# Kernel tuning notes

Measured on AMD Instinct MI355X. Metric: run time of the kernel, lower is better.

Reference implementation:

```python
import jax, jax.numpy as jnp
import numpy as np

N = 50000
NEG_SLOPE = 0.2  # PyG GATConv default negative_slope


def gat_conv(x, src, dst, W, a_src, a_dst, b, heads, out_dim, concat):
    # x: [N, F_in]; W: [F_in, heads*out_dim]; a_src/a_dst: [heads, out_dim]
    h = (x @ W).reshape(N, heads, out_dim)                      # [N,H,D]
    alpha_src = jnp.einsum('nhd,hd->nh', h, a_src)              # [N,H]
    alpha_dst = jnp.einsum('nhd,hd->nh', h, a_dst)              # [N,H]
    e = jax.nn.leaky_relu(alpha_src[src] + alpha_dst[dst], NEG_SLOPE)  # [E,H]
    # segment softmax over incoming edges of each destination node
    m = jax.ops.segment_max(e, dst, num_segments=N)             # [N,H]
    ex = jnp.exp(e - m[dst])
    denom = jax.ops.segment_sum(ex, dst, num_segments=N)        # [N,H]
    alpha = ex / (denom[dst] + 1e-16)                           # [E,H]
    msg = h[src] * alpha[:, :, None]                            # [E,H,D]
    out = jax.ops.segment_sum(msg, dst, num_segments=N)         # [N,H,D]
    out = out.reshape(N, heads * out_dim) if concat else out.mean(axis=1)
    return out + b


def setup_inputs() -> dict:
    key = jax.random.key(0)
    ks = jax.random.split(key, 14)
    E = 800000
    IN, HID, H, LAT = 128, 64, 4, 64

    def glorot(k, shape):
        fan = shape[0] + shape[-1]
        return jax.random.uniform(k, shape, jnp.float32, -1.0, 1.0) * np.sqrt(6.0 / fan)

    return {
        'x': jax.random.normal(ks[0], (N, IN), jnp.float32),
        'edge_index': jax.random.randint(ks[1], (2, E), 0, N, jnp.int64),
        'W1': glorot(ks[2], (IN, H * HID)),
        'a_src1': glorot(ks[3], (H, HID)),
        'a_dst1': glorot(ks[4], (H, HID)),
        'b1': jnp.zeros((H * HID,), jnp.float32),
        'W_mu': glorot(ks[5], (H * HID, LAT)),
        'a_src_mu': glorot(ks[6], (1, LAT)),
        'a_dst_mu': glorot(ks[7], (1, LAT)),
        'b_mu': jnp.zeros((LAT,), jnp.float32),
        'W_ls': glorot(ks[8], (H * HID, LAT)),
        'a_src_ls': glorot(ks[9], (1, LAT)),
        'a_dst_ls': glorot(ks[10], (1, LAT)),
        'b_ls': jnp.zeros((LAT,), jnp.float32),
    }


def reference(x, edge_index, W1, a_src1, a_dst1, b1,
              W_mu, a_src_mu, a_dst_mu, b_mu,
              W_ls, a_src_ls, a_dst_ls, b_ls):
    # PyG GATConv adds self-loops by default
    loops = jnp.arange(N, dtype=edge_index.dtype)
    src = jnp.concatenate([edge_index[0], loops])
    dst = jnp.concatenate([edge_index[1], loops])

    h = jax.nn.relu(gat_conv(x, src, dst, W1, a_src1, a_dst1, b1, 4, 64, True))
    mu = gat_conv(h, src, dst, W_mu, a_src_mu, a_dst_mu, b_mu, 1, 64, False)
    logstd = gat_conv(h, src, dst, W_ls, a_src_ls, a_dst_ls, b_ls, 1, 64, False)
    return (mu, logstd)
```

## Files before the change

### kernel.cpp

```cpp
#include <hip/hip_runtime.h>
#include <hip/hip_bf16.h>

#define NNODES 50000
#define MT 3125
#define NB 196
#define BCAP 5248
typedef __hip_bfloat16 bf16;
typedef __attribute__((ext_vector_type(8))) short bf16x8;
typedef __attribute__((ext_vector_type(4))) float f32x4;

__device__ __forceinline__ void unpack2(unsigned w, float& lo, float& hi){
  lo = __uint_as_float(w << 16);
  hi = __uint_as_float(w & 0xffff0000u);
}
__device__ __forceinline__ short f2bf(float f){
  union { __hip_bfloat16 h; short s; } u; u.h = __float2bfloat16(f); return u.s;
}
__device__ __forceinline__ float lrelu(float v){ return v > 0.f ? v : 0.2f * v; }

__global__ __launch_bounds__(256)
void cvt_w_k(const float* __restrict__ W1, const float* __restrict__ Wmu,
             const float* __restrict__ Wls, bf16x8* __restrict__ Bp1,
             bf16x8* __restrict__ Bp2){
  int t = blockIdx.x * 256 + threadIdx.x;
  if (t < 4096){
    int lane = t & 63, ct = (t >> 6) & 15, kt = t >> 10;
    int k0 = kt * 32 + (lane >> 4) * 8, col = ct * 16 + (lane & 15);
    bf16x8 o;
    #pragma unroll
    for (int j = 0; j < 8; j++) o[j] = f2bf(W1[(size_t)(k0 + j) * 256 + col]);
    Bp1[t] = o;
  } else if (t < 8192){
    int u = t - 4096;
    int lane = u & 63, ct = (u >> 6) & 7, kt = u >> 9;
    int k0 = kt * 32 + (lane >> 4) * 8, col = ct * 16 + (lane & 15);
    const float* W = (col < 64) ? Wmu : Wls;
    int cc = col & 63;
    bf16x8 o;
    #pragma unroll
    for (int j = 0; j < 8; j++) o[j] = f2bf(W[(size_t)(k0 + j) * 64 + cc]);
    Bp2[u] = o;
  }
}

__global__ __launch_bounds__(256)
void gemm1_mfma(const float* __restrict__ x, const bf16x8* __restrict__ Bp,
                const float* __restrict__ aS, const float* __restrict__ aD,
                bf16* __restrict__ Y, float* __restrict__ as1, float* __restrict__ ad1){
  int rt = blockIdx.x;
  int w = threadIdx.x >> 6, lane = threadIdx.x & 63;
  const float* xr = x + (size_t)(rt * 16 + (lane & 15)) * 128 + (lane >> 4) * 8;
  f32x4 z = {0.f, 0.f, 0.f, 0.f};
  f32x4 acc[4] = {z, z, z, z};
  for (int kt = 0; kt < 4; kt++){
    float4 v0 = *(const float4*)(xr + kt * 32);
    float4 v1 = *(const float4*)(xr + kt * 32 + 4);
    bf16x8 a;
    a[0] = f2bf(v0.x); a[1] = f2bf(v0.y); a[2] = f2bf(v0.z); a[3] = f2bf(v0.w);
    a[4] = f2bf(v1.x); a[5] = f2bf(v1.y); a[6] = f2bf(v1.z); a[7] = f2bf(v1.w);
    #pragma unroll
    for (int c = 0; c < 4; c++){
      bf16x8 b = Bp[(size_t)(kt * 16 + w * 4 + c) * 64 + lane];
      acc[c] = __builtin_amdgcn_mfma_f32_16x16x32_bf16(a, b, acc[c], 0, 0, 0);
    }
  }
  int row0 = rt * 16 + (lane >> 4) * 4;
  #pragma unroll
  for (int c = 0; c < 4; c++){
    int col = w * 64 + c * 16 + (lane & 15);
    #pragma unroll
    for (int i = 0; i < 4; i++)
      Y[(size_t)(row0 + i) * 256 + col] = __float2bfloat16(acc[c][i]);
  }
  float aSv[4], aDv[4];
  #pragma unroll
  for (int c = 0; c < 4; c++){
    int col = c * 16 + (lane & 15);
    aSv[c] = aS[w * 64 + col];
    aDv[c] = aD[w * 64 + col];
  }
  #pragma unroll
  for (int i = 0; i < 4; i++){
    float s1 = 0.f, s2 = 0.f;
    #pragma unroll
    for (int c = 0; c < 4; c++){
      s1 = fmaf(acc[c][i], aSv[c], s1);
      s2 = fmaf(acc[c][i], aDv[c], s2);
    }
    #pragma unroll
    for (int o = 1; o < 16; o <<= 1){
      s1 += __shfl_xor(s1, o);
      s2 += __shfl_xor(s2, o);
    }
    if ((lane & 15) == 0){
      int node = row0 + i;
      as1[node * 4 + w] = s1;
      ad1[node * 4 + w] = s2;
    }
  }
}

__global__ __launch_bounds__(256)
void gemm2_mfma(const bf16x8* __restrict__ Ap, const bf16x8* __restrict__ Bp,
                const float* __restrict__ aSmu, const float* __restrict__ aDmu,
                const float* __restrict__ aSls, const float* __restrict__ aDls,
                bf16* __restrict__ Y2,
                float* __restrict__ as2m, float* __restrict__ ad2m,
                float* __restrict__ as2l, float* __restrict__ ad2l){
  int w = threadIdx.x >> 6, lane = threadIdx.x & 63;
  int rt = blockIdx.x * 4 + w;
  if (rt >= MT) return;
  f32x4 z = {0.f, 0.f, 0.f, 0.f};
  f32x4 acc[8] = {z, z, z, z, z, z, z, z};
  for (int kt = 0; kt < 8; kt++){
    bf16x8 a = Ap[(size_t)(rt * 8 + kt) * 64 + lane];
    #pragma unroll
    for (int c = 0; c < 8; c++){
      bf16x8 b = Bp[(size_t)(kt * 8 + c) * 64 + lane];
      acc[c] = __builtin_amdgcn_mfma_f32_16x16x32_bf16(a, b, acc[c], 0, 0, 0);
    }
  }
  int row0 = rt * 16 + (lane >> 4) * 4;
  #pragma unroll
  for (int c = 0; c < 4; c++){
    int col = c * 16 + (lane & 15);
    #pragma unroll
    for (int i = 0; i < 4; i++){
      Y2[(size_t)(row0 + i) * 128 + col]       = __float2bfloat16(acc[c][i]);
      Y2[(size_t)(row0 + i) * 128 + 64 + col]  = __float2bfloat16(acc[4 + c][i]);
    }
  }
  float aSm[4], aDm[4], aSl[4], aDl[4];
  #pragma unroll
  for (int c = 0; c < 4; c++){
    int col = c * 16 + (lane & 15);
    aSm[c] = aSmu[col]; aDm[c] = aDmu[col];
    aSl[c] = aSls[col]; aDl[c] = aDls[col];
  }
  #pragma unroll
  for (int i = 0; i < 4; i++){
    float s1 = 0.f, s2 = 0.f, s3 = 0.f, s4 = 0.f;
    #pragma unroll
    for (int c = 0; c < 4; c++){
      s1 = fmaf(acc[c][i], aSm[c], s1);
      s2 = fmaf(acc[c][i], aDm[c], s2);
      s3 = fmaf(acc[4 + c][i], aSl[c], s3);
      s4 = fmaf(acc[4 + c][i], aDl[c], s4);
    }
    #pragma unroll
    for (int o = 1; o < 16; o <<= 1){
      s1 += __shfl_xor(s1, o);
      s2 += __shfl_xor(s2, o);
      s3 += __shfl_xor(s3, o);
      s4 += __shfl_xor(s4, o);
    }
    if ((lane & 15) == 0){
      int node = row0 + i;
      as2m[node] = s1; ad2m[node] = s2;
      as2l[node] = s3; ad2l[node] = s4;
    }
  }
}

__global__ __launch_bounds__(256)
void bscat_k(const int* __restrict__ ei, int E0, int Etot,
             int* __restrict__ bcnt, unsigned* __restrict__ buck){
  __shared__ int lh[NB];
  __shared__ int lbase[NB];
  for (int i = threadIdx.x; i < NB; i += 256) lh[i] = 0;
  __syncthreads();
  int base = blockIdx.x * 1024 + threadIdx.x;
  int sA[4], dA[4], rA[4];
  #pragma unroll
  for (int q = 0; q < 4; q++){
    int e = base + q * 256;
    sA[q] = -1;
    if (e < Etot){
      int s, d;
      if (e < E0){ s = ei[e]; d = ei[E0 + e]; } else { s = d = e - E0; }
      sA[q] = s; dA[q] = d;
      rA[q] = atomicAdd(&lh[d >> 8], 1);
    }
  }
  __syncthreads();
  for (int i = threadIdx.x; i < NB; i += 256)
    lbase[i] = lh[i] ? atomicAdd(&bcnt[i], lh[i]) : 0;
  __syncthreads();
  #pragma unroll
  for (int q = 0; q < 4; q++){
    if (sA[q] >= 0){
      int bk = dA[q] >> 8;
      buck[(size_t)bk * BCAP + lbase[bk] + rA[q]] =
          ((unsigned)(dA[q] & 255) << 16) | (unsigned)sA[q];
    }
  }
}

__global__ __launch_bounds__(256)
void bcsr_k(const unsigned* __restrict__ buck, const int* __restrict__ bcnt,
            int* __restrict__ offs, int* __restrict__ srcs, int n, int total){
  int b = blockIdx.x;
  __shared__ int eh[256];
  __shared__ int buf[256];
  int t = threadIdx.x;
  int bv = (t < NB) ? bcnt[t] : 0;
  buf[t] = bv; __syncthreads();
  int bacc = bv;
  for (int off = 1; off < 256; off <<= 1){
    int x = (t >= off) ? buf[t - off] : 0;
    __syncthreads();
    bacc += x; buf[t] = bacc; __syncthreads();
  }
  int gbase = (b == 0) ? 0 : buf[b - 1];
  int cntb  = bcnt[b];
  const unsigned* slab = buck + (size_t)b * BCAP;
  __syncthreads();
  eh[t] = 0;
  __syncthreads();
  for (int j = t; j < cntb; j += 256)
    atomicAdd(&eh[(slab[j] >> 16) & 255], 1);
  __syncthreads();
  int v = eh[t];
  buf[t] = v; __syncthreads();
  int acc = v;
  for (int off = 1; off < 256; off <<= 1){
    int x = (t >= off) ? buf[t - off] : 0;
    __syncthreads();
    acc += x; buf[t] = acc; __syncthreads();
  }
  int loff = acc - v;
  int node = b * 256 + t;
  if (node < n) offs[node] = gbase + loff;
  if (b == NB - 1 && t == 0) offs[n] = total;
  __syncthreads();
  eh[t] = loff;
  __syncthreads();
  for (int j = t; j < cntb; j += 256){
    unsigned val = slab[j];
    int dlo = (val >> 16) & 255;
    int rank = atomicAdd(&eh[dlo], 1);
    srcs[gbase + rank] = (int)(val & 0xffffu);
  }
}

__global__ __launch_bounds__(128)
void gat_aggr1_k(const int* __restrict__ offs, const int* __restrict__ srcs,
                 const float* __restrict__ as, const float* __restrict__ ad,
                 const bf16* __restrict__ h, const float* __restrict__ b,
                 bf16x8* __restrict__ Ap2, int n){
  int node = blockIdx.x * 2 + (threadIdx.x >> 6);
  if (node >= n) return;
  int lane = threadIdx.x & 63;
  int beg = offs[node], end = offs[node + 1];
  int hA = lane >> 4, iA = lane & 15;
  float advA = ad[node * 4 + hA];
  float m = -1e30f;
  for (int j = beg + iA; j < end; j += 16)
    m = fmaxf(m, lrelu(as[srcs[j] * 4 + hA] + advA));
  #pragma unroll
  for (int o = 1; o < 16; o <<= 1) m = fmaxf(m, __shfl_xor(m, o));
  int hP = (lane >> 3) & 3, oct = lane & 7, slot = lane >> 5;
  float mP   = __shfl(m, hP * 16);
  float advP = __shfl(advA, hP * 16);
  float s = 0.f;
  float acc[8];
  #pragma unroll
  for (int i = 0; i < 8; i++) acc[i] = 0.f;
  float p_cur = 0.f;
  uint4 dw_cur = make_uint4(0u, 0u, 0u, 0u);
  {
    int j = beg + slot;
    if (j < end){
      int si = srcs[j];
      dw_cur = *(const uint4*)(h + (size_t)si * 256 + hP * 64 + oct * 8);
      float e = lrelu(as[si * 4 + hP] + advP);
      p_cur = __expf(e - mP);
    }
  }
  for (int j0 = beg; j0 < end; j0 += 2){
    int jn = j0 + 2 + slot;
    float p_nxt = 0.f;
    uint4 dw_nxt = make_uint4(0u, 0u, 0u, 0u);
    if (jn < end){
      int si = srcs[jn];
      dw_nxt = *(const uint4*)(h + (size_t)si * 256 + hP * 64 + oct * 8);
      float e = lrelu(as[si * 4 + hP] + advP);
      p_nxt = __expf(e - mP);
    }
    s += p_cur;
    float lo, hi;
    unpack2(dw_cur.x, lo, hi); acc[0] = fmaf(lo, p_cur, acc[0]); acc[1] = fmaf(hi, p_cur, acc[1]);
    unpack2(dw_cur.y, lo, hi); acc[2] = fmaf(lo, p_cur, acc[2]); acc[3] = fmaf(hi, p_cur, acc[3]);
    unpack2(dw_cur.z, lo, hi); acc[4] = fmaf(lo, p_cur, acc[4]); acc[5] = fmaf(hi, p_cur, acc[5]);
    unpack2(dw_cur.w, lo, hi); acc[6] = fmaf(lo, p_cur, acc[6]); acc[7] = fmaf(hi, p_cur, acc[7]);
    p_cur = p_nxt;
    dw_cur = dw_nxt;
  }
  s += __shfl_xor(s, 32);
  #pragma unroll
  for (int i = 0; i < 8; i++) acc[i] += __shfl_xor(acc[i], 32);
  if (lane < 32){
    float inv = 1.f / (s + 1e-16f);
    bf16x8 o;
    #pragma unroll
    for (int i = 0; i < 8; i++){
      float vv = acc[i] * inv + b[lane * 8 + i];
      o[i] = f2bf(vv > 0.f ? vv : 0.f);
    }
    int kt = lane >> 2, g = lane & 3;
    int rt = node >> 4, r = node & 15;
    Ap2[(size_t)(rt * 8 + kt) * 64 + g * 16 + r] = o;
  }
}

__global__ __launch_bounds__(128)
void gat_aggr2_k(const int* __restrict__ offs, const int* __restrict__ srcs,
                 const float* __restrict__ as2m, const float* __restrict__ ad2m,
                 const float* __restrict__ as2l, const float* __restrict__ ad2l,
                 const bf16* __restrict__ h2,
                 const float* __restrict__ bmu, const float* __restrict__ bls,
                 float* __restrict__ outmu, float* __restrict__ outls, int n){
  int node = blockIdx.x * 2 + (threadIdx.x >> 6);
  if (node >= n) return;
  int lane = threadIdx.x & 63;
  int beg = offs[node], end = offs[node + 1];
  const float* asA = (lane >= 32) ? as2l : as2m;
  float advA = ((lane >= 32) ? ad2l : ad2m)[node];
  int iA = lane & 31;
  float m = -1e30f;
  for (int j = beg + iA; j < end; j += 32)
    m = fmaxf(m, lrelu(asA[srcs[j]] + advA));
  #pragma unroll
  for (int o = 1; o < 32; o <<= 1) m = fmaxf(m, __shfl_xor(m, o));
  int br = (lane >> 3) & 1, oct = lane & 7, slot = lane >> 4;
  float mP   = __shfl(m, br * 32);
  float advP = __shfl(advA, br * 32);
  const float* asP = br ? as2l : as2m;
  float s = 0.f;
  float acc[8];
  #pragma unroll
  for (int i = 0; i < 8; i++) acc[i] = 0.f;
  #pragma unroll 8
  for (int j0 = beg; j0 < end; j0 += 4){
    int j = j0 + slot;
    if (j < end){
      int si = srcs[j];
      float e = lrelu(asP[si] + advP);
      float p = __expf(e - mP);
      s += p;
      uint4 dw = *(const uint4*)(h2 + (size_t)si * 128 + br * 64 + oct * 8);
      float lo, hi;
      unpack2(dw.x, lo, hi); acc[0] = fmaf(lo, p, acc[0]); acc[1] = fmaf(hi, p, acc[1]);
      unpack2(dw.y, lo, hi); acc[2] = fmaf(lo, p, acc[2]); acc[3] = fmaf(hi, p, acc[3]);
      unpack2(dw.z, lo, hi); acc[4] = fmaf(lo, p, acc[4]); acc[5] = fmaf(hi, p, acc[5]);
      unpack2(dw.w, lo, hi); acc[6] = fmaf(lo, p, acc[6]); acc[7] = fmaf(hi, p, acc[7]);
    }
  }
  #pragma unroll
  for (int off = 16; off <= 32; off <<= 1){
    s += __shfl_xor(s, off);
    #pragma unroll
    for (int i = 0; i < 8; i++) acc[i] += __shfl_xor(acc[i], off);
  }
  if (lane < 16){
    float inv = 1.f / (s + 1e-16f);
    const float* bb = (lane >= 8) ? bls : bmu;
    float* out = (lane >= 8) ? outls : outmu;
    float v[8];
    #pragma unroll
    for (int i = 0; i < 8; i++) v[i] = acc[i] * inv + bb[oct * 8 + i];
    float* op = out + (size_t)node * 64 + oct * 8;
    *(float4*)op       = make_float4(v[0], v[1], v[2], v[3]);
    *(float4*)(op + 4) = make_float4(v[4], v[5], v[6], v[7]);
  }
}

extern "C" void kernel_launch(void* const* d_in, const int* in_sizes, int n_in,
                              void* d_out, int out_size, void* d_ws, size_t ws_size,
                              hipStream_t stream){
  const float* x    = (const float*)d_in[0];
  const int*   ei   = (const int*)d_in[1];
  const float* W1   = (const float*)d_in[2];
  const float* aS1  = (const float*)d_in[3];
  const float* aD1  = (const float*)d_in[4];
  const float* b1   = (const float*)d_in[5];
  const float* Wmu  = (const float*)d_in[6];
  const float* aSmu = (const float*)d_in[7];
  const float* aDmu = (const float*)d_in[8];
  const float* bmu  = (const float*)d_in[9];
  const float* Wls  = (const float*)d_in[10];
  const float* aSls = (const float*)d_in[11];
  const float* aDls = (const float*)d_in[12];
  const float* bls  = (const float*)d_in[13];

  const int N    = NNODES;
  const int E0   = in_sizes[1] / 2;
  const int Etot = E0 + N;

  float* ws = (float*)d_ws;
  bf16x8* Ap2  = (bf16x8*)(ws);
  bf16*   h1bf = (bf16*)(ws + 6400000);
  bf16*   h2   = (bf16*)(ws + 12800000);
  float*  as1  = ws + 16000000;
  float*  ad1  = ws + 16200000;
  float*  as2m = ws + 16400000;
  float*  ad2m = ws + 16450000;
  float*  as2l = ws + 16500000;
  float*  ad2l = ws + 16550000;
  int*      offs  = (int*)(ws + 16600000);
  int*      srcs  = (int*)(ws + 16650016);
  unsigned* buck  = (unsigned*)(ws + 17500016);
  int*      bcnt  = (int*)(ws + 18528640);
  bf16x8*   Bp1   = (bf16x8*)(ws + 18528912);
  bf16x8*   Bp2   = (bf16x8*)(ws + 18545296);

  float* outmu = (float*)d_out;
  float* outls = (float*)d_out + 3200000;

  const int egrid4 = (Etot + 1023) / 1024;

  hipMemsetAsync(bcnt, 0, 256 * sizeof(int), stream);
  bscat_k<<<egrid4, 256, 0, stream>>>(ei, E0, Etot, bcnt, buck);
  bcsr_k<<<NB, 256, 0, stream>>>(buck, bcnt, offs, srcs, N, Etot);

  cvt_w_k<<<32, 256, 0, stream>>>(W1, Wmu, Wls, Bp1, Bp2);

  gemm1_mfma<<<MT, 256, 0, stream>>>(x, Bp1, aS1, aD1, h1bf, as1, ad1);
  gat_aggr1_k<<<(N + 1) / 2, 128, 0, stream>>>(offs, srcs, as1, ad1, h1bf, b1, Ap2, N);

  gemm2_mfma<<<(MT + 3) / 4, 256, 0, stream>>>(Ap2, Bp2, aSmu, aDmu, aSls, aDls,
                                               h2, as2m, ad2m, as2l, ad2l);
  gat_aggr2_k<<<(N + 1) / 2, 128, 0, stream>>>(offs, srcs, as2m, ad2m, as2l, ad2l,
                                               h2, bmu, bls, outmu, outls, N);
}
```

Before: 213.3 us.

## Fold weight conversion into bucket scatter and use grid-stride aggregation kernels

Merges the weight bf16 conversion kernel into the edge-bucketing kernel as extra blocks, removing one launch. Both aggregation kernels become persistent grid-stride loops over nodes with a fixed grid of 4096 blocks instead of one block per two nodes. The software-pipelined prefetch in the layer-1 aggregation is replaced with a simpler unrolled loop. The unrolled loop may expose less load latency hiding than the explicit double buffering, and a fixed grid can balance uneven node degrees less well.

```diff
diff --git a/kernel.cpp b/kernel.cpp
--- a/kernel.cpp
+++ b/kernel.cpp
@@ -17,31 +17,6 @@
   union { __hip_bfloat16 h; short s; } u; u.h = __float2bfloat16(f); return u.s;
 }
 __device__ __forceinline__ float lrelu(float v){ return v > 0.f ? v : 0.2f * v; }
-
-__global__ __launch_bounds__(256)
-void cvt_w_k(const float* __restrict__ W1, const float* __restrict__ Wmu,
-             const float* __restrict__ Wls, bf16x8* __restrict__ Bp1,
-             bf16x8* __restrict__ Bp2){
-  int t = blockIdx.x * 256 + threadIdx.x;
-  if (t < 4096){
-    int lane = t & 63, ct = (t >> 6) & 15, kt = t >> 10;
-    int k0 = kt * 32 + (lane >> 4) * 8, col = ct * 16 + (lane & 15);
-    bf16x8 o;
-    #pragma unroll
-    for (int j = 0; j < 8; j++) o[j] = f2bf(W1[(size_t)(k0 + j) * 256 + col]);
-    Bp1[t] = o;
-  } else if (t < 8192){
-    int u = t - 4096;
-    int lane = u & 63, ct = (u >> 6) & 7, kt = u >> 9;
-    int k0 = kt * 32 + (lane >> 4) * 8, col = ct * 16 + (lane & 15);
-    const float* W = (col < 64) ? Wmu : Wls;
-    int cc = col & 63;
-    bf16x8 o;
-    #pragma unroll
-    for (int j = 0; j < 8; j++) o[j] = f2bf(W[(size_t)(k0 + j) * 64 + cc]);
-    Bp2[u] = o;
-  }
-}
 
 __global__ __launch_bounds__(256)
 void gemm1_mfma(const float* __restrict__ x, const bf16x8* __restrict__ Bp,
@@ -164,7 +139,32 @@
 
 __global__ __launch_bounds__(256)
 void bscat_k(const int* __restrict__ ei, int E0, int Etot,
-             int* __restrict__ bcnt, unsigned* __restrict__ buck){
+             int* __restrict__ bcnt, unsigned* __restrict__ buck, int sblocks,
+             const float* __restrict__ W1, const float* __restrict__ Wmu,
+             const float* __restrict__ Wls, bf16x8* __restrict__ Bp1,
+             bf16x8* __restrict__ Bp2){
+  if (blockIdx.x >= sblocks){
+    int t = (blockIdx.x - sblocks) * 256 + threadIdx.x;
+    if (t < 4096){
+      int lane = t & 63, ct = (t >> 6) & 15, kt = t >> 10;
+      int k0 = kt * 32 + (lane >> 4) * 8, col = ct * 16 + (lane & 15);
+      bf16x8 o;
+      #pragma unroll
+      for (int j = 0; j < 8; j++) o[j] = f2bf(W1[(size_t)(k0 + j) * 256 + col]);
+      Bp1[t] = o;
+    } else if (t < 8192){
+      int u = t - 4096;
+      int lane = u & 63, ct = (u >> 6) & 7, kt = u >> 9;
+      int k0 = kt * 32 + (lane >> 4) * 8, col = ct * 16 + (lane & 15);
+      const float* W = (col < 64) ? Wmu : Wls;
+      int cc = col & 63;
+      bf16x8 o;
+      #pragma unroll
+      for (int j = 0; j < 8; j++) o[j] = f2bf(W[(size_t)(k0 + j) * 64 + cc]);
+      Bp2[u] = o;
+    }
+    return;
+  }
   __shared__ int lh[NB];
   __shared__ int lbase[NB];
   for (int i = threadIdx.x; i < NB; i += 256) lh[i] = 0;
@@ -248,68 +248,54 @@
                  const float* __restrict__ as, const float* __restrict__ ad,
                  const bf16* __restrict__ h, const float* __restrict__ b,
                  bf16x8* __restrict__ Ap2, int n){
-  int node = blockIdx.x * 2 + (threadIdx.x >> 6);
-  if (node >= n) return;
   int lane = threadIdx.x & 63;
-  int beg = offs[node], end = offs[node + 1];
   int hA = lane >> 4, iA = lane & 15;
-  float advA = ad[node * 4 + hA];
-  float m = -1e30f;
-  for (int j = beg + iA; j < end; j += 16)
-    m = fmaxf(m, lrelu(as[srcs[j] * 4 + hA] + advA));
-  #pragma unroll
-  for (int o = 1; o < 16; o <<= 1) m = fmaxf(m, __shfl_xor(m, o));
   int hP = (lane >> 3) & 3, oct = lane & 7, slot = lane >> 5;
-  float mP   = __shfl(m, hP * 16);
-  float advP = __shfl(advA, hP * 16);
-  float s = 0.f;
-  float acc[8];
-  #pragma unroll
-  for (int i = 0; i < 8; i++) acc[i] = 0.f;
-  float p_cur = 0.f;
-  uint4 dw_cur = make_uint4(0u, 0u, 0u, 0u);
-  {
-    int j = beg + slot;
-    if (j < end){
-      int si = srcs[j];
-      dw_cur = *(const uint4*)(h + (size_t)si * 256 + hP * 64 + oct * 8);
-      float e = lrelu(as[si * 4 + hP] + advP);
-      p_cur = __expf(e - mP);
-    }
-  }
-  for (int j0 = beg; j0 < end; j0 += 2){
-    int jn = j0 + 2 + slot;
-    float p_nxt = 0.f;
-    uint4 dw_nxt = make_uint4(0u, 0u, 0u, 0u);
-    if (jn < end){
-      int si = srcs[jn];
-      dw_nxt = *(const uint4*)(h + (size_t)si * 256 + hP * 64 + oct * 8);
-      float e = lrelu(as[si * 4 + hP] + advP);
-      p_nxt = __expf(e - mP);
-    }
-    s += p_cur;
-    float lo, hi;
-    unpack2(dw_cur.x, lo, hi); acc[0] = fmaf(lo, p_cur, acc[0]); acc[1] = fmaf(hi, p_cur, acc[1]);
-    unpack2(dw_cur.y, lo, hi); acc[2] = fmaf(lo, p_cur, acc[2]); acc[3] = fmaf(hi, p_cur, acc[3]);
-    unpack2(dw_cur.z, lo, hi); acc[4] = fmaf(lo, p_cur, acc[4]); acc[5] = fmaf(hi, p_cur, acc[5]);
-    unpack2(dw_cur.w, lo, hi); acc[6] = fmaf(lo, p_cur, acc[6]); acc[7] = fmaf(hi, p_cur, acc[7]);
-    p_cur = p_nxt;
-    dw_cur = dw_nxt;
-  }
-  s += __shfl_xor(s, 32);
-  #pragma unroll
-  for (int i = 0; i < 8; i++) acc[i] += __shfl_xor(acc[i], 32);
-  if (lane < 32){
-    float inv = 1.f / (s + 1e-16f);
-    bf16x8 o;
-    #pragma unroll
-    for (int i = 0; i < 8; i++){
-      float vv = acc[i] * inv + b[lane * 8 + i];
-      o[i] = f2bf(vv > 0.f ? vv : 0.f);
-    }
-    int kt = lane >> 2, g = lane & 3;
-    int rt = node >> 4, r = node & 15;
-    Ap2[(size_t)(rt * 8 + kt) * 64 + g * 16 + r] = o;
+  for (int node = blockIdx.x * 2 + (threadIdx.x >> 6); node < n; node += gridDim.x * 2){
+    int beg = offs[node], end = offs[node + 1];
+    float advA = ad[node * 4 + hA];
+    float m = -1e30f;
+    for (int j = beg + iA; j < end; j += 16)
+      m = fmaxf(m, lrelu(as[srcs[j] * 4 + hA] + advA));
+    #pragma unroll
+    for (int o = 1; o < 16; o <<= 1) m = fmaxf(m, __shfl_xor(m, o));
+    float mP   = __shfl(m, hP * 16);
+    float advP = __shfl(advA, hP * 16);
+    float s = 0.f;
+    float acc[8];
+    #pragma unroll
+    for (int i = 0; i < 8; i++) acc[i] = 0.f;
+    #pragma unroll 8
+    for (int j0 = beg; j0 < end; j0 += 2){
+      int j = j0 + slot;
+      if (j < end){
+        int si = srcs[j];
+        float e = lrelu(as[si * 4 + hP] + advP);
+        float p = __expf(e - mP);
+        s += p;
+        uint4 dw = *(const uint4*)(h + (size_t)si * 256 + hP * 64 + oct * 8);
+        float lo, hi;
+        unpack2(dw.x, lo, hi); acc[0] = fmaf(lo, p, acc[0]); acc[1] = fmaf(hi, p, acc[1]);
+        unpack2(dw.y, lo, hi); acc[2] = fmaf(lo, p, acc[2]); acc[3] = fmaf(hi, p, acc[3]);
+        unpack2(dw.z, lo, hi); acc[4] = fmaf(lo, p, acc[4]); acc[5] = fmaf(hi, p, acc[5]);
+        unpack2(dw.w, lo, hi); acc[6] = fmaf(lo, p, acc[6]); acc[7] = fmaf(hi, p, acc[7]);
+      }
+    }
+    s += __shfl_xor(s, 32);
+    #pragma unroll
+    for (int i = 0; i < 8; i++) acc[i] += __shfl_xor(acc[i], 32);
+    if (lane < 32){
+      float inv = 1.f / (s + 1e-16f);
+      bf16x8 o;
+      #pragma unroll
+      for (int i = 0; i < 8; i++){
+        float vv = acc[i] * inv + b[lane * 8 + i];
+        o[i] = f2bf(vv > 0.f ? vv : 0.f);
+      }
+      int kt = lane >> 2, g = lane & 3;
+      int rt = node >> 4, r = node & 15;
+      Ap2[(size_t)(rt * 8 + kt) * 64 + g * 16 + r] = o;
+    }
   }
 }
 
@@ -320,58 +306,59 @@
                  const bf16* __restrict__ h2,
                  const float* __restrict__ bmu, const float* __restrict__ bls,
                  float* __restrict__ outmu, float* __restrict__ outls, int n){
-  int node = blockIdx.x * 2 + (threadIdx.x >> 6);
-  if (node >= n) return;
   int lane = threadIdx.x & 63;
-  int beg = offs[node], end = offs[node + 1];
+  int iA = lane & 31;
+  int br = (lane >> 3) & 1, oct = lane & 7, slot = lane >> 4;
   const float* asA = (lane >= 32) ? as2l : as2m;
-  float advA = ((lane >= 32) ? ad2l : ad2m)[node];
-  int iA = lane & 31;
-  float m = -1e30f;
-  for (int j = beg + iA; j < end; j += 32)
-    m = fmaxf(m, lrelu(asA[srcs[j]] + advA));
-  #pragma unroll
-  for (int o = 1; o < 32; o <<= 1) m = fmaxf(m, __shfl_xor(m, o));
-  int br = (lane >> 3) & 1, oct = lane & 7, slot = lane >> 4;
-  float mP   = __shfl(m, br * 32);
-  float advP = __shfl(advA, br * 32);
+  const float* adA = (lane >= 32) ? ad2l : ad2m;
   const float* asP = br ? as2l : as2m;
-  float s = 0.f;
-  float acc[8];
-  #pragma unroll
-  for (int i = 0; i < 8; i++) acc[i] = 0.f;
-  #pragma unroll 8
-  for (int j0 = beg; j0 < end; j0 += 4){
-    int j = j0 + slot;
-    if (j < end){
-      int si = srcs[j];
-      float e = lrelu(asP[si] + advP);
-      float p = __expf(e - mP);
-      s += p;
-      uint4 dw = *(const uint4*)(h2 + (size_t)si * 128 + br * 64 + oct * 8);
-      float lo, hi;
-      unpack2(dw.x, lo, hi); acc[0] = fmaf(lo, p, acc[0]); acc[1] = fmaf(hi, p, acc[1]);
-      unpack2(dw.y, lo, hi); acc[2] = fmaf(lo, p, acc[2]); acc[3] = fmaf(hi, p, acc[3]);
-      unpack2(dw.z, lo, hi); acc[4] = fmaf(lo, p, acc[4]); acc[5] = fmaf(hi, p, acc[5]);
-      unpack2(dw.w, lo, hi); acc[6] = fmaf(lo, p, acc[6]); acc[7] = fmaf(hi, p, acc[7]);
-    }
-  }
-  #pragma unroll
-  for (int off = 16; off <= 32; off <<= 1){
-    s += __shfl_xor(s, off);
-    #pragma unroll
-    for (int i = 0; i < 8; i++) acc[i] += __shfl_xor(acc[i], off);
-  }
-  if (lane < 16){
-    float inv = 1.f / (s + 1e-16f);
-    const float* bb = (lane >= 8) ? bls : bmu;
-    float* out = (lane >= 8) ? outls : outmu;
-    float v[8];
-    #pragma unroll
-    for (int i = 0; i < 8; i++) v[i] = acc[i] * inv + bb[oct * 8 + i];
-    float* op = out + (size_t)node * 64 + oct * 8;
-    *(float4*)op       = make_float4(v[0], v[1], v[2], v[3]);
-    *(float4*)(op + 4) = make_float4(v[4], v[5], v[6], v[7]);
+  for (int node = blockIdx.x * 2 + (threadIdx.x >> 6); node < n; node += gridDim.x * 2){
+    int beg = offs[node], end = offs[node + 1];
+    float advA = adA[node];
+    float m = -1e30f;
+    for (int j = beg + iA; j < end; j += 32)
+      m = fmaxf(m, lrelu(asA[srcs[j]] + advA));
+    #pragma unroll
+    for (int o = 1; o < 32; o <<= 1) m = fmaxf(m, __shfl_xor(m, o));
+    float mP   = __shfl(m, br * 32);
+    float advP = __shfl(advA, br * 32);
+    float s = 0.f;
+    float acc[8];
+    #pragma unroll
+    for (int i = 0; i < 8; i++) acc[i] = 0.f;
+    #pragma unroll 8
+    for (int j0 = beg; j0 < end; j0 += 4){
+      int j = j0 + slot;
+      if (j < end){
+        int si = srcs[j];
+        float e = lrelu(asP[si] + advP);
+        float p = __expf(e - mP);
+        s += p;
+        uint4 dw = *(const uint4*)(h2 + (size_t)si * 128 + br * 64 + oct * 8);
+        float lo, hi;
+        unpack2(dw.x, lo, hi); acc[0] = fmaf(lo, p, acc[0]); acc[1] = fmaf(hi, p, acc[1]);
+        unpack2(dw.y, lo, hi); acc[2] = fmaf(lo, p, acc[2]); acc[3] = fmaf(hi, p, acc[3]);
+        unpack2(dw.z, lo, hi); acc[4] = fmaf(lo, p, acc[4]); acc[5] = fmaf(hi, p, acc[5]);
+        unpack2(dw.w, lo, hi); acc[6] = fmaf(lo, p, acc[6]); acc[7] = fmaf(hi, p, acc[7]);
+      }
+    }
+    #pragma unroll
+    for (int off = 16; off <= 32; off <<= 1){
+      s += __shfl_xor(s, off);
+      #pragma unroll
+      for (int i = 0; i < 8; i++) acc[i] += __shfl_xor(acc[i], off);
+    }
+    if (lane < 16){
+      float inv = 1.f / (s + 1e-16f);
+      const float* bb = (lane >= 8) ? bls : bmu;
+      float* out = (lane >= 8) ? outls : outmu;
+      float v[8];
+      #pragma unroll
+      for (int i = 0; i < 8; i++) v[i] = acc[i] * inv + bb[oct * 8 + i];
+      float* op = out + (size_t)node * 64 + oct * 8;
+      *(float4*)op       = make_float4(v[0], v[1], v[2], v[3]);
+      *(float4*)(op + 4) = make_float4(v[4], v[5], v[6], v[7]);
+    }
   }
 }
 
@@ -420,16 +407,15 @@
   const int egrid4 = (Etot + 1023) / 1024;
 
   hipMemsetAsync(bcnt, 0, 256 * sizeof(int), stream);
-  bscat_k<<<egrid4, 256, 0, stream>>>(ei, E0, Etot, bcnt, buck);
+  bscat_k<<<egrid4 + 32, 256, 0, stream>>>(ei, E0, Etot, bcnt, buck, egrid4,
+                                           W1, Wmu, Wls, Bp1, Bp2);
   bcsr_k<<<NB, 256, 0, stream>>>(buck, bcnt, offs, srcs, N, Etot);
 
-  cvt_w_k<<<32, 256, 0, stream>>>(W1, Wmu, Wls, Bp1, Bp2);
-
   gemm1_mfma<<<MT, 256, 0, stream>>>(x, Bp1, aS1, aD1, h1bf, as1, ad1);
-  gat_aggr1_k<<<(N + 1) / 2, 128, 0, stream>>>(offs, srcs, as1, ad1, h1bf, b1, Ap2, N);
+  gat_aggr1_k<<<4096, 128, 0, stream>>>(offs, srcs, as1, ad1, h1bf, b1, Ap2, N);
 
   gemm2_mfma<<<(MT + 3) / 4, 256, 0, stream>>>(Ap2, Bp2, aSmu, aDmu, aSls, aDls,
                                                h2, as2m, ad2m, as2l, ad2l);
-  gat_aggr2_k<<<(N + 1) / 2, 128, 0, stream>>>(offs, srcs, as2m, ad2m, as2l, ad2l,
-                                               h2, bmu, bls, outmu, outls, N);
-}
+  gat_aggr2_k<<<4096, 128, 0, stream>>>(offs, srcs, as2m, ad2m, as2l, ad2l,
+                                        h2, bmu, bls, outmu, outls, N);
+}
```

Measured after the change: 212.8 us. No clear change (-0.2%).
